# Optimization experiments

Measured on AMD Instinct MI355X. Metric: run time of the kernel, lower is better.

Reference implementation:

```python
import jax, jax.numpy as jnp
import numpy as np

N = 100000      # nodes
E = 1600000     # edges (avg degree 16)
F_IN = 48       # input features
H = 64          # hidden
C = 2           # classes


def _init(key, shape, fan_in):
    return jax.random.normal(key, shape, jnp.float32) * (1.0 / np.sqrt(fan_in))


def setup_inputs() -> dict:
    key = jax.random.key(0)
    ks = jax.random.split(key, 12)
    return {
        "x": jax.random.normal(ks[0], (N, F_IN), jnp.float32),
        "edge_index": jax.random.randint(ks[1], (2, E), 0, N, dtype=jnp.int64),
        "W1l": _init(ks[2], (F_IN, H), F_IN),
        "b1l": jnp.zeros((H,), jnp.float32),
        "W1r": _init(ks[3], (F_IN, H), F_IN),
        "W2l": _init(ks[4], (H, H), H),
        "b2l": jnp.zeros((H,), jnp.float32),
        "W2r": _init(ks[5], (H, H), H),
        "Wlin1": _init(ks[6], (H, H), H),
        "blin1": jnp.zeros((H,), jnp.float32),
        "Wlin2": _init(ks[7], (H, C), H),
        "blin2": jnp.zeros((C,), jnp.float32),
    }


def _sage_conv(x, src, dst, Wl, bl, Wr, num_nodes):
    # mean aggregation of source-node features onto destination nodes
    msg = x[src]                                              # [E, F] gather
    agg = jax.ops.segment_sum(msg, dst, num_segments=num_nodes)
    cnt = jax.ops.segment_sum(jnp.ones((dst.shape[0], 1), x.dtype), dst,
                              num_segments=num_nodes)
    mean = agg / jnp.maximum(cnt, 1.0)
    # PyG SAGEConv: lin_l(aggr) + lin_r(root); bias only on lin_l
    return mean @ Wl + bl + x @ Wr


def reference(x, edge_index, W1l, b1l, W1r, W2l, b2l, W2r,
              Wlin1, blin1, Wlin2, blin2):
    src, dst = edge_index[0], edge_index[1]
    n = x.shape[0]
    h = jax.nn.sigmoid(_sage_conv(x, src, dst, W1l, b1l, W1r, n))
    h = jax.nn.sigmoid(_sage_conv(h, src, dst, W2l, b2l, W2r, n))
    # dropout(p=0.5) is identity in eval mode (self.training=False)
    h = jax.nn.sigmoid(h @ Wlin1 + blin1)
    return jax.nn.softmax(h @ Wlin2 + blin2, axis=1)
```

## Files before the change

### kernel.cpp

```cpp
#include <hip/hip_runtime.h>
#include <math.h>


#define NF1 48
#define HH 64
#define BKT_SHIFT 8
#define BKT_SZ (1 << BKT_SHIFT)
#define BCAP 4800
#define EPB 16

typedef __attribute__((ext_vector_type(8))) short short8v;
typedef __attribute__((ext_vector_type(4))) float float4v;

__device__ __forceinline__ float sigmoidf_(float v) {
  return 1.0f / (1.0f + __expf(-v));
}
__device__ __forceinline__ float bflo(unsigned w) {
  union { unsigned u; float f; } c; c.u = w << 16; return c.f;
}
__device__ __forceinline__ float bfhi(unsigned w) {
  union { unsigned u; float f; } c; c.u = w & 0xffff0000u; return c.f;
}
__device__ __forceinline__ unsigned short f2bf(float f) {
  union { float f; unsigned u; } c; c.f = f;
  unsigned r = c.u + 0x7fffu + ((c.u >> 16) & 1u);
  return (unsigned short)(r >> 16);
}

template <int K>
__global__ __launch_bounds__(256, 4) void fused_bin_gemm(
    const int* __restrict__ ei, int* __restrict__ cursor,
    unsigned* __restrict__ bins, int E, int NB,
    const float* __restrict__ X, const float* __restrict__ Wl,
    const float* __restrict__ Wr, const float* __restrict__ bias,
    unsigned short* __restrict__ t_out, float* __restrict__ r_out,
    int n_nodes, int abk, int gemmb) {
  __shared__ __align__(16) char smem[3 * 64 * 72 * 2];

  if ((int)blockIdx.x < abk) {
    int* hist = (int*)smem;
    int* gbase = hist + 512;
    for (int i = threadIdx.x; i < NB; i += 256) hist[i] = 0;
    __syncthreads();
    int base_e = blockIdx.x * (256 * EPB) + threadIdx.x;
    unsigned pk[EPB];
    int bk[EPB], rk[EPB];
#pragma unroll
    for (int k = 0; k < EPB; k++) {
      int e = base_e + k * 256;
      bk[k] = -1;
      if (e < E) {
        int s = ei[e], d = ei[E + e];
        int b = d >> BKT_SHIFT;
        pk[k] = ((unsigned)(d & (BKT_SZ - 1)) << 23) | (unsigned)s;
        bk[k] = b;
        rk[k] = atomicAdd(&hist[b], 1);
      }
    }
    __syncthreads();
    for (int i = threadIdx.x; i < NB; i += 256) {
      int c = hist[i];
      gbase[i] = (c > 0) ? atomicAdd(&cursor[i], c) : 0;
    }
    __syncthreads();
#pragma unroll
    for (int k = 0; k < EPB; k++) {
      if (bk[k] >= 0) {
        int pos = gbase[bk[k]] + rk[k];
        bins[(size_t)bk[k] * BCAP + pos] = pk[k];
      }
    }
    return;
  }

  short(*sA)[72] = (short(*)[72])smem;
  short(*sWl)[72] = (short(*)[72])(smem + 9216);
  short(*sWr)[72] = (short(*)[72])(smem + 18432);
  int gbid = (int)blockIdx.x - abk;
  int lane = threadIdx.x & 63, wv = threadIdx.x >> 6;
  int l15 = lane & 15, kq = lane >> 4;

  for (int i = threadIdx.x; i < 64 * 64; i += 256) {
    int k = i >> 6, j = i & 63;
    short vl = 0, vr = 0;
    if (k < K) {
      vl = (short)f2bf(Wl[k * 64 + j]);
      vr = (short)f2bf(Wr[k * 64 + j]);
    }
    sWl[j][k] = vl;
    sWr[j][k] = vr;
  }
  if (K < 64) {
    constexpr int PADW = (64 - K) / 2;
    for (int i = threadIdx.x; i < 64 * PADW; i += 256) {
      int row = i / PADW, p = i % PADW;
      *(unsigned*)&sA[row][K + 2 * p] = 0u;
    }
  }
  float bcol[4];
#pragma unroll
  for (int c = 0; c < 4; c++) bcol[c] = bias[c * 16 + l15];

  for (int nbase = gbid * 64; nbase < n_nodes; nbase += gemmb * 64) {
    __syncthreads();
    for (int i = threadIdx.x; i < 64 * (K / 4); i += 256) {
      int row = i / (K / 4), c4 = i % (K / 4);
      int rr = nbase + row;
      if (rr >= n_nodes) rr = n_nodes - 1;
      float4 xv = ((const float4*)(X + (size_t)rr * K))[c4];
      unsigned lo = ((unsigned)f2bf(xv.y) << 16) | (unsigned)f2bf(xv.x);
      unsigned hi = ((unsigned)f2bf(xv.w) << 16) | (unsigned)f2bf(xv.z);
      uint2 pk2 = {lo, hi};
      *(uint2*)&sA[row][c4 * 4] = pk2;
    }
    __syncthreads();

    float4v acc_t[4], acc_r[4];
#pragma unroll
    for (int c = 0; c < 4; c++) {
      acc_t[c] = (float4v){0.0f, 0.0f, 0.0f, 0.0f};
      acc_r[c] = (float4v){bcol[c], bcol[c], bcol[c], bcol[c]};
    }
#pragma unroll
    for (int s = 0; s < 2; s++) {
      short8v af = *(const short8v*)&sA[wv * 16 + l15][s * 32 + kq * 8];
#pragma unroll
      for (int c = 0; c < 4; c++) {
        short8v bl = *(const short8v*)&sWl[c * 16 + l15][s * 32 + kq * 8];
        short8v br = *(const short8v*)&sWr[c * 16 + l15][s * 32 + kq * 8];
        acc_t[c] = __builtin_amdgcn_mfma_f32_16x16x32_bf16(af, bl, acc_t[c], 0, 0, 0);
        acc_r[c] = __builtin_amdgcn_mfma_f32_16x16x32_bf16(af, br, acc_r[c], 0, 0, 0);
      }
    }
#pragma unroll
    for (int c = 0; c < 4; c++) {
      int j = c * 16 + l15;
#pragma unroll
      for (int g = 0; g < 4; g++) {
        int node = nbase + wv * 16 + kq * 4 + g;
        if (node < n_nodes) {
          t_out[(size_t)node * HH + j] = f2bf(acc_t[c][g]);
          r_out[(size_t)node * HH + j] = acc_r[c][g];
        }
      }
    }
  }
}

__global__ __launch_bounds__(256) void build_csr2(
    const unsigned* __restrict__ bins, const int* __restrict__ cursor,
    int* __restrict__ rp, int* __restrict__ csr, int n_nodes, int E, int NB) {
  __shared__ int hist[BKT_SZ];
  __shared__ int aa[BKT_SZ], bb[BKT_SZ];
  __shared__ int cur[BKT_SZ];
  int b = blockIdx.x;
  int tid = threadIdx.x;
  int node0 = b << BKT_SHIFT;
  int cnt = cursor[b];
  const unsigned* bp = bins + (size_t)b * BCAP;

  int part = 0;
  for (int i = tid; i < b; i += 256) part += cursor[i];
  aa[tid] = part;
  __syncthreads();
  for (int off = 128; off > 0; off >>= 1) {
    if (tid < off) aa[tid] += aa[tid + off];
    __syncthreads();
  }
  int gb = aa[0];
  __syncthreads();

  hist[tid] = 0;
  __syncthreads();
  for (int i = tid; i < cnt; i += 256) {
    atomicAdd(&hist[bp[i] >> 23], 1);
  }
  __syncthreads();
  int v = hist[tid];
  aa[tid] = v;
  __syncthreads();
  int* s = aa;
  int* d = bb;
  for (int off = 1; off < BKT_SZ; off <<= 1) {
    int t = s[tid] + ((tid >= off) ? s[tid - off] : 0);
    d[tid] = t;
    __syncthreads();
    int* tmp = s; s = d; d = tmp;
  }
  int loc = s[tid] - v;
  int node = node0 + tid;
  if (node < n_nodes) rp[node] = gb + loc;
  if (b == NB - 1 && tid == 0) rp[n_nodes] = E;
  cur[tid] = gb + loc;
  __syncthreads();
  for (int i = tid; i < cnt; i += 256) {
    unsigned p = bp[i];
    int dl = (int)(p >> 23);
    int pos = atomicAdd(&cur[dl], 1);
    csr[pos] = (int)(p & 0x7FFFFFu);
  }
}

template <int K>
__global__ __launch_bounds__(256, 4) void gemm_mfma(
    const float* __restrict__ X, const float* __restrict__ Wl,
    const float* __restrict__ Wr, const float* __restrict__ bias,
    unsigned short* __restrict__ t_out, float* __restrict__ r_out,
    int n_nodes) {
  __shared__ short sA[64][72];
  __shared__ short sWl[64][72];
  __shared__ short sWr[64][72];
  int lane = threadIdx.x & 63, wv = threadIdx.x >> 6;
  int l15 = lane & 15, kq = lane >> 4;

  for (int i = threadIdx.x; i < 64 * 64; i += 256) {
    int k = i >> 6, j = i & 63;
    short vl = 0, vr = 0;
    if (k < K) {
      vl = (short)f2bf(Wl[k * 64 + j]);
      vr = (short)f2bf(Wr[k * 64 + j]);
    }
    sWl[j][k] = vl;
    sWr[j][k] = vr;
  }
  if (K < 64) {
    constexpr int PADW = (64 - K) / 2;
    for (int i = threadIdx.x; i < 64 * PADW; i += 256) {
      int row = i / PADW, p = i % PADW;
      *(unsigned*)&sA[row][K + 2 * p] = 0u;
    }
  }
  float bcol[4];
#pragma unroll
  for (int c = 0; c < 4; c++) bcol[c] = bias[c * 16 + l15];

  for (int nbase = blockIdx.x * 64; nbase < n_nodes; nbase += gridDim.x * 64) {
    __syncthreads();
    for (int i = threadIdx.x; i < 64 * (K / 4); i += 256) {
      int row = i / (K / 4), c4 = i % (K / 4);
      int rr = nbase + row;
      if (rr >= n_nodes) rr = n_nodes - 1;
      float4 xv = ((const float4*)(X + (size_t)rr * K))[c4];
      unsigned lo = ((unsigned)f2bf(xv.y) << 16) | (unsigned)f2bf(xv.x);
      unsigned hi = ((unsigned)f2bf(xv.w) << 16) | (unsigned)f2bf(xv.z);
      uint2 pk = {lo, hi};
      *(uint2*)&sA[row][c4 * 4] = pk;
    }
    __syncthreads();

    float4v acc_t[4], acc_r[4];
#pragma unroll
    for (int c = 0; c < 4; c++) {
      acc_t[c] = (float4v){0.0f, 0.0f, 0.0f, 0.0f};
      acc_r[c] = (float4v){bcol[c], bcol[c], bcol[c], bcol[c]};
    }
#pragma unroll
    for (int s = 0; s < 2; s++) {
      short8v af = *(const short8v*)&sA[wv * 16 + l15][s * 32 + kq * 8];
#pragma unroll
      for (int c = 0; c < 4; c++) {
        short8v bl = *(const short8v*)&sWl[c * 16 + l15][s * 32 + kq * 8];
        short8v br = *(const short8v*)&sWr[c * 16 + l15][s * 32 + kq * 8];
        acc_t[c] = __builtin_amdgcn_mfma_f32_16x16x32_bf16(af, bl, acc_t[c], 0, 0, 0);
        acc_r[c] = __builtin_amdgcn_mfma_f32_16x16x32_bf16(af, br, acc_r[c], 0, 0, 0);
      }
    }
#pragma unroll
    for (int c = 0; c < 4; c++) {
      int j = c * 16 + l15;
#pragma unroll
      for (int g = 0; g < 4; g++) {
        int node = nbase + wv * 16 + kq * 4 + g;
        if (node < n_nodes) {
          t_out[(size_t)node * HH + j] = f2bf(acc_t[c][g]);
          r_out[(size_t)node * HH + j] = acc_r[c][g];
        }
      }
    }
  }
}

__global__ __launch_bounds__(256) void agg_sig(
    const unsigned short* __restrict__ t, const float* __restrict__ r,
    const int* __restrict__ rp, const int* __restrict__ csr,
    float* __restrict__ h, int n_nodes) {
  int grp = threadIdx.x >> 4;
  int q = threadIdx.x & 15;
  int node = blockIdx.x * 16 + grp;
  if (node >= n_nodes) return;
  int rs = rp[node], re = rp[node + 1];
  int deg = re - rs;
  const uint2* tb = (const uint2*)t + q;

  float a0 = 0, a1 = 0, a2 = 0, a3 = 0;
  int j = rs;
  for (; j + 7 < re; j += 8) {
    uint2 u0 = tb[(size_t)csr[j + 0] * 16];
    uint2 u1 = tb[(size_t)csr[j + 1] * 16];
    uint2 u2 = tb[(size_t)csr[j + 2] * 16];
    uint2 u3 = tb[(size_t)csr[j + 3] * 16];
    uint2 u4 = tb[(size_t)csr[j + 4] * 16];
    uint2 u5 = tb[(size_t)csr[j + 5] * 16];
    uint2 u6 = tb[(size_t)csr[j + 6] * 16];
    uint2 u7 = tb[(size_t)csr[j + 7] * 16];
    a0 += ((bflo(u0.x) + bflo(u1.x)) + (bflo(u2.x) + bflo(u3.x))) +
          ((bflo(u4.x) + bflo(u5.x)) + (bflo(u6.x) + bflo(u7.x)));
    a1 += ((bfhi(u0.x) + bfhi(u1.x)) + (bfhi(u2.x) + bfhi(u3.x))) +
          ((bfhi(u4.x) + bfhi(u5.x)) + (bfhi(u6.x) + bfhi(u7.x)));
    a2 += ((bflo(u0.y) + bflo(u1.y)) + (bflo(u2.y) + bflo(u3.y))) +
          ((bflo(u4.y) + bflo(u5.y)) + (bflo(u6.y) + bflo(u7.y)));
    a3 += ((bfhi(u0.y) + bfhi(u1.y)) + (bfhi(u2.y) + bfhi(u3.y))) +
          ((bfhi(u4.y) + bfhi(u5.y)) + (bfhi(u6.y) + bfhi(u7.y)));
  }
  if (j + 3 < re) {
    uint2 u0 = tb[(size_t)csr[j + 0] * 16];
    uint2 u1 = tb[(size_t)csr[j + 1] * 16];
    uint2 u2 = tb[(size_t)csr[j + 2] * 16];
    uint2 u3 = tb[(size_t)csr[j + 3] * 16];
    a0 += (bflo(u0.x) + bflo(u1.x)) + (bflo(u2.x) + bflo(u3.x));
    a1 += (bfhi(u0.x) + bfhi(u1.x)) + (bfhi(u2.x) + bfhi(u3.x));
    a2 += (bflo(u0.y) + bflo(u1.y)) + (bflo(u2.y) + bflo(u3.y));
    a3 += (bfhi(u0.y) + bfhi(u1.y)) + (bfhi(u2.y) + bfhi(u3.y));
    j += 4;
  }
  for (; j < re; j++) {
    uint2 u = tb[(size_t)csr[j] * 16];
    a0 += bflo(u.x);
    a1 += bfhi(u.x);
    a2 += bflo(u.y);
    a3 += bfhi(u.y);
  }

  float inv = 1.0f / fmaxf((float)deg, 1.0f);
  float4 rv = ((const float4*)(r + (size_t)node * HH))[q];
  float4 o;
  o.x = sigmoidf_(a0 * inv + rv.x);
  o.y = sigmoidf_(a1 * inv + rv.y);
  o.z = sigmoidf_(a2 * inv + rv.z);
  o.w = sigmoidf_(a3 * inv + rv.w);
  ((float4*)(h + (size_t)node * HH))[q] = o;
}

__global__ __launch_bounds__(512, 4) void head_k(
    const float* __restrict__ h2,
    const float* __restrict__ Wlin1, const float* __restrict__ blin1,
    const float* __restrict__ Wlin2, const float* __restrict__ blin2,
    float* __restrict__ out, int n_nodes) {
  __shared__ float sx[64][HH];
  __shared__ float sh3[64][HH];
  __shared__ float sw2[HH * 2];
  int wv = threadIdx.x >> 6, lane = threadIdx.x & 63;

  float w1[HH];
#pragma unroll
  for (int k = 0; k < HH; k++) w1[k] = Wlin1[k * HH + lane];
  float bv = blin1[lane];
  if (threadIdx.x < HH * 2) sw2[threadIdx.x] = Wlin2[threadIdx.x];
  float sb20 = blin2[0], sb21 = blin2[1];

  for (int nbase = blockIdx.x * 64; nbase < n_nodes; nbase += gridDim.x * 64) {
    __syncthreads();
    for (int i = threadIdx.x; i < 64 * (HH / 4); i += 512) {
      int row = i >> 4, c4 = i & 15;
      int rr = nbase + row;
      if (rr >= n_nodes) rr = n_nodes - 1;
      ((float4*)sx[row])[c4] = ((const float4*)(h2 + (size_t)rr * HH))[c4];
    }
    __syncthreads();

    float acc[8];
#pragma unroll
    for (int m = 0; m < 8; m++) acc[m] = bv;
#pragma unroll
    for (int k = 0; k < HH; k += 4) {
#pragma unroll
      for (int m = 0; m < 8; m++) {
        float4 a = *(const float4*)&sx[wv * 8 + m][k];
        acc[m] += a.x * w1[k] + a.y * w1[k + 1] + a.z * w1[k + 2] + a.w * w1[k + 3];
      }
    }
#pragma unroll
    for (int m = 0; m < 8; m++) sh3[wv * 8 + m][lane] = sigmoidf_(acc[m]);
    __syncthreads();

    int node_l = threadIdx.x >> 3;
    int sub = threadIdx.x & 7;
    float l0 = 0.0f, l1 = 0.0f;
#pragma unroll
    for (int kk = 0; kk < 8; kk++) {
      int k = sub * 8 + kk;
      float v = sh3[node_l][k];
      l0 += v * sw2[k * 2 + 0];
      l1 += v * sw2[k * 2 + 1];
    }
    l0 += __shfl_xor(l0, 1); l1 += __shfl_xor(l1, 1);
    l0 += __shfl_xor(l0, 2); l1 += __shfl_xor(l1, 2);
    l0 += __shfl_xor(l0, 4); l1 += __shfl_xor(l1, 4);
    int node = nbase + node_l;
    if (sub == 0 && node < n_nodes) {
      l0 += sb20;
      l1 += sb21;
      float mx = fmaxf(l0, l1);
      float p0 = __expf(l0 - mx), p1 = __expf(l1 - mx);
      float s = 1.0f / (p0 + p1);
      float2 o2 = {p0 * s, p1 * s};
      ((float2*)out)[node] = o2;
    }
  }
}

extern "C" void kernel_launch(void* const* d_in, const int* in_sizes, int n_in,
                              void* d_out, int out_size, void* d_ws, size_t ws_size,
                              hipStream_t stream) {
  const float* x     = (const float*)d_in[0];
  const int*   ei    = (const int*)d_in[1];
  const float* W1l   = (const float*)d_in[2];
  const float* b1l   = (const float*)d_in[3];
  const float* W1r   = (const float*)d_in[4];
  const float* W2l   = (const float*)d_in[5];
  const float* b2l   = (const float*)d_in[6];
  const float* W2r   = (const float*)d_in[7];
  const float* Wlin1 = (const float*)d_in[8];
  const float* blin1 = (const float*)d_in[9];
  const float* Wlin2 = (const float*)d_in[10];
  const float* blin2 = (const float*)d_in[11];
  float* out = (float*)d_out;

  int n = in_sizes[0] / NF1;
  int E = in_sizes[1] / 2;
  int NB = (n + BKT_SZ - 1) >> BKT_SHIFT;

  int* cursor = (int*)d_ws;
  int* rp     = cursor + NB;
  int* csr    = rp + n + 1;
  size_t off = (size_t)(NB + n + 1 + E) * sizeof(int);
  off = (off + 255) & ~(size_t)255;
  unsigned short* tbuf = (unsigned short*)((char*)d_ws + off);
  off += (size_t)n * HH * sizeof(unsigned short);
  off = (off + 255) & ~(size_t)255;
  float* rbuf = (float*)((char*)d_ws + off);
  off += (size_t)n * HH * sizeof(float);
  off = (off + 255) & ~(size_t)255;
  float* hbuf = (float*)((char*)d_ws + off);
  unsigned* bins = (unsigned*)hbuf;

  hipMemsetAsync(cursor, 0, (size_t)NB * sizeof(int), stream);

  int abk = (E + 256 * EPB - 1) / (256 * EPB);
  int gemmb = (n + 63) / 64;
  if (gemmb > 1024) gemmb = 1024;
  int aggb = (n + 15) / 16;
  int headb = (n + 63) / 64;
  if (headb > 1024) headb = 1024;

  fused_bin_gemm<NF1><<<abk + gemmb, 256, 0, stream>>>(
      ei, cursor, bins, E, NB, x, W1l, W1r, b1l, tbuf, rbuf, n, abk, gemmb);

  build_csr2<<<NB, 256, 0, stream>>>(bins, cursor, rp, csr, n, E, NB);

  agg_sig<<<aggb, 256, 0, stream>>>(tbuf, rbuf, rp, csr, hbuf, n);

  gemm_mfma<HH><<<gemmb, 256, 0, stream>>>(hbuf, W2l, W2r, b2l, tbuf, rbuf, n);
  agg_sig<<<aggb, 256, 0, stream>>>(tbuf, rbuf, rp, csr, hbuf, n);

  head_k<<<headb, 512, 0, stream>>>(hbuf, Wlin1, blin1, Wlin2, blin2, out, n);
}
```

Baseline: 170.5 us.

## Fuse neighbor aggregation into layer-2 GEMM and head kernels

Merges the first aggregation+sigmoid into the layer-2 MFMA GEMM kernel, writing the hidden activations straight to shared memory as bf16. The second aggregation is merged into the head MLP kernel, and the root-term buffer r2 is now stored in bf16. This removes two kernel launches and the full-size fp32 h round trips through global memory. In exchange, the gather phase now runs in GEMM-sized grids capped at 1024 blocks with fewer nodes in flight per wave, which may reduce latency hiding for the irregular gathers, and there is some extra bf16 rounding.

```diff
diff --git a/kernel.cpp b/kernel.cpp
--- a/kernel.cpp
+++ b/kernel.cpp
@@ -201,98 +201,10 @@
   }
 }
 
-template <int K>
-__global__ __launch_bounds__(256, 4) void gemm_mfma(
-    const float* __restrict__ X, const float* __restrict__ Wl,
-    const float* __restrict__ Wr, const float* __restrict__ bias,
-    unsigned short* __restrict__ t_out, float* __restrict__ r_out,
-    int n_nodes) {
-  __shared__ short sA[64][72];
-  __shared__ short sWl[64][72];
-  __shared__ short sWr[64][72];
-  int lane = threadIdx.x & 63, wv = threadIdx.x >> 6;
-  int l15 = lane & 15, kq = lane >> 4;
-
-  for (int i = threadIdx.x; i < 64 * 64; i += 256) {
-    int k = i >> 6, j = i & 63;
-    short vl = 0, vr = 0;
-    if (k < K) {
-      vl = (short)f2bf(Wl[k * 64 + j]);
-      vr = (short)f2bf(Wr[k * 64 + j]);
-    }
-    sWl[j][k] = vl;
-    sWr[j][k] = vr;
-  }
-  if (K < 64) {
-    constexpr int PADW = (64 - K) / 2;
-    for (int i = threadIdx.x; i < 64 * PADW; i += 256) {
-      int row = i / PADW, p = i % PADW;
-      *(unsigned*)&sA[row][K + 2 * p] = 0u;
-    }
-  }
-  float bcol[4];
-#pragma unroll
-  for (int c = 0; c < 4; c++) bcol[c] = bias[c * 16 + l15];
-
-  for (int nbase = blockIdx.x * 64; nbase < n_nodes; nbase += gridDim.x * 64) {
-    __syncthreads();
-    for (int i = threadIdx.x; i < 64 * (K / 4); i += 256) {
-      int row = i / (K / 4), c4 = i % (K / 4);
-      int rr = nbase + row;
-      if (rr >= n_nodes) rr = n_nodes - 1;
-      float4 xv = ((const float4*)(X + (size_t)rr * K))[c4];
-      unsigned lo = ((unsigned)f2bf(xv.y) << 16) | (unsigned)f2bf(xv.x);
-      unsigned hi = ((unsigned)f2bf(xv.w) << 16) | (unsigned)f2bf(xv.z);
-      uint2 pk = {lo, hi};
-      *(uint2*)&sA[row][c4 * 4] = pk;
-    }
-    __syncthreads();
-
-    float4v acc_t[4], acc_r[4];
-#pragma unroll
-    for (int c = 0; c < 4; c++) {
-      acc_t[c] = (float4v){0.0f, 0.0f, 0.0f, 0.0f};
-      acc_r[c] = (float4v){bcol[c], bcol[c], bcol[c], bcol[c]};
-    }
-#pragma unroll
-    for (int s = 0; s < 2; s++) {
-      short8v af = *(const short8v*)&sA[wv * 16 + l15][s * 32 + kq * 8];
-#pragma unroll
-      for (int c = 0; c < 4; c++) {
-        short8v bl = *(const short8v*)&sWl[c * 16 + l15][s * 32 + kq * 8];
-        short8v br = *(const short8v*)&sWr[c * 16 + l15][s * 32 + kq * 8];
-        acc_t[c] = __builtin_amdgcn_mfma_f32_16x16x32_bf16(af, bl, acc_t[c], 0, 0, 0);
-        acc_r[c] = __builtin_amdgcn_mfma_f32_16x16x32_bf16(af, br, acc_r[c], 0, 0, 0);
-      }
-    }
-#pragma unroll
-    for (int c = 0; c < 4; c++) {
-      int j = c * 16 + l15;
-#pragma unroll
-      for (int g = 0; g < 4; g++) {
-        int node = nbase + wv * 16 + kq * 4 + g;
-        if (node < n_nodes) {
-          t_out[(size_t)node * HH + j] = f2bf(acc_t[c][g]);
-          r_out[(size_t)node * HH + j] = acc_r[c][g];
-        }
-      }
-    }
-  }
-}
-
-__global__ __launch_bounds__(256) void agg_sig(
-    const unsigned short* __restrict__ t, const float* __restrict__ r,
-    const int* __restrict__ rp, const int* __restrict__ csr,
-    float* __restrict__ h, int n_nodes) {
-  int grp = threadIdx.x >> 4;
-  int q = threadIdx.x & 15;
-  int node = blockIdx.x * 16 + grp;
-  if (node >= n_nodes) return;
-  int rs = rp[node], re = rp[node + 1];
-  int deg = re - rs;
-  const uint2* tb = (const uint2*)t + q;
-
-  float a0 = 0, a1 = 0, a2 = 0, a3 = 0;
+__device__ __forceinline__ void gather4(const uint2* __restrict__ tb,
+                                        const int* __restrict__ csr,
+                                        int rs, int re,
+                                        float& a0, float& a1, float& a2, float& a3) {
   int j = rs;
   for (; j + 7 < re; j += 8) {
     uint2 u0 = tb[(size_t)csr[j + 0] * 16];
@@ -330,26 +242,99 @@
     a2 += bflo(u.y);
     a3 += bfhi(u.y);
   }
-
-  float inv = 1.0f / fmaxf((float)deg, 1.0f);
-  float4 rv = ((const float4*)(r + (size_t)node * HH))[q];
-  float4 o;
-  o.x = sigmoidf_(a0 * inv + rv.x);
-  o.y = sigmoidf_(a1 * inv + rv.y);
-  o.z = sigmoidf_(a2 * inv + rv.z);
-  o.w = sigmoidf_(a3 * inv + rv.w);
-  ((float4*)(h + (size_t)node * HH))[q] = o;
-}
-
-__global__ __launch_bounds__(512, 4) void head_k(
-    const float* __restrict__ h2,
+}
+
+__global__ __launch_bounds__(256, 4) void fused_agg_gemm(
+    const unsigned short* __restrict__ t1, const float* __restrict__ r1,
+    const int* __restrict__ rp, const int* __restrict__ csr,
+    const float* __restrict__ W2l, const float* __restrict__ W2r,
+    const float* __restrict__ b2l,
+    unsigned short* __restrict__ t2, unsigned short* __restrict__ r2,
+    int n_nodes, int gemmb) {
+  __shared__ short sA[64][72];
+  __shared__ short sWl[64][72];
+  __shared__ short sWr[64][72];
+  int lane = threadIdx.x & 63, wv = threadIdx.x >> 6;
+  int l15 = lane & 15, kq = lane >> 4;
+  int grp = threadIdx.x >> 4, q = threadIdx.x & 15;
+
+  for (int i = threadIdx.x; i < 64 * 64; i += 256) {
+    int k = i >> 6, j = i & 63;
+    sWl[j][k] = (short)f2bf(W2l[k * 64 + j]);
+    sWr[j][k] = (short)f2bf(W2r[k * 64 + j]);
+  }
+  float bcol[4];
+#pragma unroll
+  for (int c = 0; c < 4; c++) bcol[c] = b2l[c * 16 + l15];
+
+  for (int nbase = blockIdx.x * 64; nbase < n_nodes; nbase += gemmb * 64) {
+    __syncthreads();
+#pragma unroll
+    for (int p = 0; p < 4; p++) {
+      int row = p * 16 + grp;
+      int node = nbase + row;
+      int nn = node < n_nodes ? node : n_nodes - 1;
+      int rs = rp[nn], re = rp[nn + 1];
+      int deg = re - rs;
+      const uint2* tb = (const uint2*)t1 + q;
+      float a0 = 0, a1 = 0, a2 = 0, a3 = 0;
+      gather4(tb, csr, rs, re, a0, a1, a2, a3);
+      float inv = 1.0f / fmaxf((float)deg, 1.0f);
+      float4 rv = ((const float4*)(r1 + (size_t)nn * HH))[q];
+      float h0 = sigmoidf_(a0 * inv + rv.x);
+      float h1v = sigmoidf_(a1 * inv + rv.y);
+      float h2v = sigmoidf_(a2 * inv + rv.z);
+      float h3v = sigmoidf_(a3 * inv + rv.w);
+      unsigned lo = ((unsigned)f2bf(h1v) << 16) | (unsigned)f2bf(h0);
+      unsigned hi = ((unsigned)f2bf(h3v) << 16) | (unsigned)f2bf(h2v);
+      uint2 pk = {lo, hi};
+      *(uint2*)&sA[row][q * 4] = pk;
+    }
+    __syncthreads();
+
+    float4v acc_t[4], acc_r[4];
+#pragma unroll
+    for (int c = 0; c < 4; c++) {
+      acc_t[c] = (float4v){0.0f, 0.0f, 0.0f, 0.0f};
+      acc_r[c] = (float4v){bcol[c], bcol[c], bcol[c], bcol[c]};
+    }
+#pragma unroll
+    for (int s = 0; s < 2; s++) {
+      short8v af = *(const short8v*)&sA[wv * 16 + l15][s * 32 + kq * 8];
+#pragma unroll
+      for (int c = 0; c < 4; c++) {
+        short8v bl = *(const short8v*)&sWl[c * 16 + l15][s * 32 + kq * 8];
+        short8v br = *(const short8v*)&sWr[c * 16 + l15][s * 32 + kq * 8];
+        acc_t[c] = __builtin_amdgcn_mfma_f32_16x16x32_bf16(af, bl, acc_t[c], 0, 0, 0);
+        acc_r[c] = __builtin_amdgcn_mfma_f32_16x16x32_bf16(af, br, acc_r[c], 0, 0, 0);
+      }
+    }
+#pragma unroll
+    for (int c = 0; c < 4; c++) {
+      int j = c * 16 + l15;
+#pragma unroll
+      for (int g = 0; g < 4; g++) {
+        int node = nbase + wv * 16 + kq * 4 + g;
+        if (node < n_nodes) {
+          t2[(size_t)node * HH + j] = f2bf(acc_t[c][g]);
+          r2[(size_t)node * HH + j] = f2bf(acc_r[c][g]);
+        }
+      }
+    }
+  }
+}
+
+__global__ __launch_bounds__(512, 4) void fused_agg_head(
+    const unsigned short* __restrict__ t2, const unsigned short* __restrict__ r2,
+    const int* __restrict__ rp, const int* __restrict__ csr,
     const float* __restrict__ Wlin1, const float* __restrict__ blin1,
     const float* __restrict__ Wlin2, const float* __restrict__ blin2,
-    float* __restrict__ out, int n_nodes) {
+    float* __restrict__ out, int n_nodes, int headb) {
   __shared__ float sx[64][HH];
   __shared__ float sh3[64][HH];
   __shared__ float sw2[HH * 2];
   int wv = threadIdx.x >> 6, lane = threadIdx.x & 63;
+  int grp = threadIdx.x >> 4, q = threadIdx.x & 15;
 
   float w1[HH];
 #pragma unroll
@@ -358,13 +343,26 @@
   if (threadIdx.x < HH * 2) sw2[threadIdx.x] = Wlin2[threadIdx.x];
   float sb20 = blin2[0], sb21 = blin2[1];
 
-  for (int nbase = blockIdx.x * 64; nbase < n_nodes; nbase += gridDim.x * 64) {
-    __syncthreads();
-    for (int i = threadIdx.x; i < 64 * (HH / 4); i += 512) {
-      int row = i >> 4, c4 = i & 15;
-      int rr = nbase + row;
-      if (rr >= n_nodes) rr = n_nodes - 1;
-      ((float4*)sx[row])[c4] = ((const float4*)(h2 + (size_t)rr * HH))[c4];
+  for (int nbase = blockIdx.x * 64; nbase < n_nodes; nbase += headb * 64) {
+    __syncthreads();
+#pragma unroll
+    for (int p = 0; p < 2; p++) {
+      int row = p * 32 + grp;
+      int node = nbase + row;
+      int nn = node < n_nodes ? node : n_nodes - 1;
+      int rs = rp[nn], re = rp[nn + 1];
+      int deg = re - rs;
+      const uint2* tb = (const uint2*)t2 + q;
+      float a0 = 0, a1 = 0, a2 = 0, a3 = 0;
+      gather4(tb, csr, rs, re, a0, a1, a2, a3);
+      float inv = 1.0f / fmaxf((float)deg, 1.0f);
+      uint2 ru = ((const uint2*)(r2 + (size_t)nn * HH))[q];
+      float4 o;
+      o.x = sigmoidf_(a0 * inv + bflo(ru.x));
+      o.y = sigmoidf_(a1 * inv + bfhi(ru.x));
+      o.z = sigmoidf_(a2 * inv + bflo(ru.y));
+      o.w = sigmoidf_(a3 * inv + bfhi(ru.y));
+      *(float4*)&sx[row][q * 4] = o;
     }
     __syncthreads();
 
@@ -435,33 +433,35 @@
   int* csr    = rp + n + 1;
   size_t off = (size_t)(NB + n + 1 + E) * sizeof(int);
   off = (off + 255) & ~(size_t)255;
-  unsigned short* tbuf = (unsigned short*)((char*)d_ws + off);
+  unsigned short* t1 = (unsigned short*)((char*)d_ws + off);
   off += (size_t)n * HH * sizeof(unsigned short);
   off = (off + 255) & ~(size_t)255;
-  float* rbuf = (float*)((char*)d_ws + off);
+  float* r1 = (float*)((char*)d_ws + off);
   off += (size_t)n * HH * sizeof(float);
   off = (off + 255) & ~(size_t)255;
-  float* hbuf = (float*)((char*)d_ws + off);
-  unsigned* bins = (unsigned*)hbuf;
+  unsigned short* t2 = (unsigned short*)((char*)d_ws + off);
+  off += (size_t)n * HH * sizeof(unsigned short);
+  off = (off + 255) & ~(size_t)255;
+  unsigned short* r2 = (unsigned short*)((char*)d_ws + off);
+  unsigned* bins = (unsigned*)t2;
 
   hipMemsetAsync(cursor, 0, (size_t)NB * sizeof(int), stream);
 
   int abk = (E + 256 * EPB - 1) / (256 * EPB);
   int gemmb = (n + 63) / 64;
   if (gemmb > 1024) gemmb = 1024;
-  int aggb = (n + 15) / 16;
   int headb = (n + 63) / 64;
   if (headb > 1024) headb = 1024;
 
   fused_bin_gemm<NF1><<<abk + gemmb, 256, 0, stream>>>(
-      ei, cursor, bins, E, NB, x, W1l, W1r, b1l, tbuf, rbuf, n, abk, gemmb);
+      ei, cursor, bins, E, NB, x, W1l, W1r, b1l, t1, r1, n, abk, gemmb);
 
   build_csr2<<<NB, 256, 0, stream>>>(bins, cursor, rp, csr, n, E, NB);
 
-  agg_sig<<<aggb, 256, 0, stream>>>(tbuf, rbuf, rp, csr, hbuf, n);
-
-  gemm_mfma<HH><<<gemmb, 256, 0, stream>>>(hbuf, W2l, W2r, b2l, tbuf, rbuf, n);
-  agg_sig<<<aggb, 256, 0, stream>>>(tbuf, rbuf, rp, csr, hbuf, n);
-
-  head_k<<<headb, 512, 0, stream>>>(hbuf, Wlin1, blin1, Wlin2, blin2, out, n);
-}
+  fused_agg_gemm<<<gemmb, 256, 0, stream>>>(t1, r1, rp, csr, W2l, W2r, b2l,
+                                            t2, r2, n, gemmb);
+
+  fused_agg_head<<<headb, 512, 0, stream>>>(t2, r2, rp, csr,
+                                            Wlin1, blin1, Wlin2, blin2,
+                                            out, n, headb);
+}
```

Measured after the change: 175.7 us. 1.03x slower.
